# Optimization experiments

Hardware: AMD Instinct MI355X
Metric: run time of the kernel (lower is better)

## Reference

```python
import jax, jax.numpy as jnp
import numpy as np

N_USERS = 50000
N_ITEMS = 100000
N_NODES = N_USERS + N_ITEMS
N_EDGES = 2000000
EMBED = 64
N_LAYERS = 3
BATCH = 8192
NEG_SLOPE = 0.01  # torch LeakyReLU default
EPS = 1e-12       # torch F.normalize default


def setup_inputs() -> dict:
    key = jax.random.key(0)
    ks = jax.random.split(key, 12)
    return {
        "user_emb": jax.random.normal(ks[0], (N_USERS, EMBED), jnp.float32) * 0.1,
        "item_emb": jax.random.normal(ks[1], (N_ITEMS, EMBED), jnp.float32) * 0.1,
        "W1": jax.random.normal(ks[2], (N_LAYERS, EMBED, EMBED), jnp.float32) * 0.1,
        "b1": jax.random.normal(ks[3], (N_LAYERS, EMBED), jnp.float32) * 0.01,
        "W2": jax.random.normal(ks[4], (N_LAYERS, EMBED, EMBED), jnp.float32) * 0.1,
        "b2": jax.random.normal(ks[5], (N_LAYERS, EMBED), jnp.float32) * 0.01,
        "adj_vals": jax.random.uniform(ks[6], (N_EDGES,), jnp.float32),
        "adj_rows": jax.random.randint(ks[7], (N_EDGES,), 0, N_NODES, jnp.int32),
        "adj_cols": jax.random.randint(ks[8], (N_EDGES,), 0, N_NODES, jnp.int32),
        "u": jax.random.randint(ks[9], (BATCH,), 0, N_USERS, jnp.int32),
        "i": jax.random.randint(ks[10], (BATCH,), 0, N_ITEMS, jnp.int32),
        "j": jax.random.randint(ks[11], (BATCH,), 0, N_ITEMS, jnp.int32),
    }


def _spmm(rows, cols, vals, x):
    # sparse [N,N] @ dense [N,d] via gather + segment-sum
    return jax.ops.segment_sum(vals[:, None] * x[cols], rows, num_segments=N_NODES)


def _forward(user_emb, item_emb, W1, b1, W2, b2, adj_vals, adj_rows, adj_cols, u, i, j):
    emb = jnp.concatenate([user_emb, item_emb], axis=0)  # [N, d]
    finals = [emb]
    for l in range(N_LAYERS):
        t1e = _spmm(adj_rows, adj_cols, adj_vals, emb)        # A @ E
        t1 = t1e @ W1[l].T + b1[l]                             # Linear W1
        t2 = (emb * t1e) @ W2[l].T + b2[l]                     # Linear W2 on E (.) AE
        emb = jax.nn.leaky_relu(t1 + t2, NEG_SLOPE)
        norm = jnp.sqrt(jnp.sum(emb * emb, axis=1, keepdims=True))
        finals.append(emb / jnp.maximum(norm, EPS))
    fin = jnp.concatenate(finals, axis=1)                      # [N, d*(L+1)]
    fin_u, fin_i = fin[:N_USERS], fin[N_USERS:]
    bu, bp, bn = fin_u[u], fin_i[i], fin_i[j]
    pos_y = jnp.sum(bu * bp, axis=1)
    neg_y = jnp.sum(bu * bn, axis=1)
    return -jnp.mean(jax.nn.log_sigmoid(pos_y - neg_y))


def reference(user_emb, item_emb, W1, b1, W2, b2, adj_vals, adj_rows, adj_cols, u, i, j):
    return _forward(user_emb, item_emb, W1, b1, W2, b2, adj_vals, adj_rows, adj_cols, u, i, j)
```

## Files before the change

### kernel.cpp

```cpp
#include <hip/hip_runtime.h>
#include <hip/hip_bf16.h>
#include <math.h>

#define N_USERS 50000
#define N_ITEMS 100000
#define N_NODES 150000
#define N_EDGES 2000000
#define EMBED 64
#define N_LAYERS 3
#define BATCH 8192

#define BSHIFT 9
#define BROWS 512
#define NBKT ((N_NODES + BROWS - 1) / BROWS)
#define EPB 4096

typedef __bf16 bf16x8 __attribute__((ext_vector_type(8)));
typedef float  f32x4  __attribute__((ext_vector_type(4)));

__device__ __forceinline__ float bf2f(unsigned short u) {
    union { unsigned int i; float f; } c; c.i = ((unsigned int)u) << 16; return c.f;
}
__device__ __forceinline__ unsigned short f2bf(float f) {
    __hip_bfloat16 h = __float2bfloat16(f);
    union { __hip_bfloat16 h; unsigned short u; } c; c.h = h; return c.u;
}
__device__ __forceinline__ bf16x8 as_bf8(uint4 u) {
    union { uint4 u; bf16x8 v; } c; c.u = u; return c.v;
}
__device__ __forceinline__ void unpack8(uint4 u, float* f) {
    union { unsigned int i; float x; } c;
    c.i = u.x << 16; f[0] = c.x; c.i = u.x & 0xffff0000u; f[1] = c.x;
    c.i = u.y << 16; f[2] = c.x; c.i = u.y & 0xffff0000u; f[3] = c.x;
    c.i = u.z << 16; f[4] = c.x; c.i = u.z & 0xffff0000u; f[5] = c.x;
    c.i = u.w << 16; f[6] = c.x; c.i = u.w & 0xffff0000u; f[7] = c.x;
}
__device__ __forceinline__ bf16x8 pack8(const float* f) {
    union { unsigned short s[8]; bf16x8 v; } u;
#pragma unroll
    for (int j = 0; j < 8; j++) u.s[j] = f2bf(f[j]);
    return u.v;
}

__global__ __launch_bounds__(256) void k_tobf16(const float4* __restrict__ ue,
                                                const float4* __restrict__ ie,
                                                ushort4* __restrict__ tab) {
    int idx = blockIdx.x * 256 + threadIdx.x;
    const int TOT = N_NODES * EMBED / 4;
    const int UPART = N_USERS * EMBED / 4;
    if (idx < TOT) {
        float4 v = (idx < UPART) ? ue[idx] : ie[idx - UPART];
        ushort4 o;
        o.x = f2bf(v.x); o.y = f2bf(v.y); o.z = f2bf(v.z); o.w = f2bf(v.w);
        tab[idx] = o;
    }
}

__global__ __launch_bounds__(256) void k_wprep(const float* __restrict__ W1,
                                               const float* __restrict__ b1,
                                               const float* __restrict__ W2,
                                               const float* __restrict__ b2,
                                               unsigned short* __restrict__ Wb,
                                               float* __restrict__ bsum) {
    int idx = blockIdx.x * 256 + threadIdx.x;
    if (idx < 3 * 64 * 128) {
        int l = idx >> 13, rem = idx & 8191;
        int n = rem >> 7, k = rem & 127;
        float w = (k < 64) ? W1[l * 4096 + n * 64 + k] : W2[l * 4096 + n * 64 + (k - 64)];
        Wb[idx] = f2bf(w);
    } else if (idx < 3 * 64 * 128 + 192) {
        int t = idx - 3 * 64 * 128;
        bsum[t] = b1[t] + b2[t];
    }
}

__global__ __launch_bounds__(256) void k_bkt_count(const int* __restrict__ rows,
                                                   int* __restrict__ bkt_count) {
    __shared__ int hist[NBKT];
    int tid = threadIdx.x;
    for (int t = tid; t < NBKT; t += 256) hist[t] = 0;
    __syncthreads();
    int e = (blockIdx.x * 256 + tid) * 4;
    if (e + 3 < N_EDGES) {
        int4 r = *(const int4*)&rows[e];
        atomicAdd(&hist[r.x >> BSHIFT], 1);
        atomicAdd(&hist[r.y >> BSHIFT], 1);
        atomicAdd(&hist[r.z >> BSHIFT], 1);
        atomicAdd(&hist[r.w >> BSHIFT], 1);
    } else {
        for (int k = 0; k < 4; k++)
            if (e + k < N_EDGES) atomicAdd(&hist[rows[e + k] >> BSHIFT], 1);
    }
    __syncthreads();
    for (int t = tid; t < NBKT; t += 256)
        if (hist[t] > 0) atomicAdd(&bkt_count[t], hist[t]);
}

__global__ __launch_bounds__(512) void k_bkt_scan(const int* __restrict__ bkt_count,
                                                  int* __restrict__ bkt_base,
                                                  int* __restrict__ bkt_cursor,
                                                  int* __restrict__ row_ptr) {
    int tid = threadIdx.x;
    int x = (tid < NBKT) ? bkt_count[tid] : 0;
    int lane = tid & 63, wid = tid >> 6;
    int v = x;
    for (int o = 1; o < 64; o <<= 1) {
        int t = __shfl_up(v, o);
        if (lane >= o) v += t;
    }
    __shared__ int wsum[8];
    if (lane == 63) wsum[wid] = v;
    __syncthreads();
    int add = 0;
    for (int w = 0; w < wid; w++) add += wsum[w];
    int incl = add + v;
    int excl = incl - x;
    if (tid < NBKT) {
        bkt_base[tid]   = excl;
        bkt_cursor[tid] = excl;
    }
    if (tid == NBKT - 1) {
        bkt_base[NBKT]    = incl;
        row_ptr[N_NODES]  = incl;
    }
}

__global__ __launch_bounds__(256) void k_bucketA(const int* __restrict__ rows,
                                                 const int* __restrict__ cols,
                                                 const float* __restrict__ vals,
                                                 int* __restrict__ bkt_cursor,
                                                 int4* __restrict__ bucketed) {
    __shared__ int sr[EPB];
    __shared__ int sc[EPB];
    __shared__ int sv[EPB];
    __shared__ int hist[NBKT];
    __shared__ int cbase[NBKT];
    int tid = threadIdx.x;
    int e0 = blockIdx.x * EPB;
    int cnt = N_EDGES - e0; if (cnt > EPB) cnt = EPB;

    for (int i = tid; i < cnt; i += 256) {
        sr[i] = rows[e0 + i];
        sc[i] = cols[e0 + i];
        sv[i] = __float_as_int(vals[e0 + i]);
    }
    for (int t = tid; t < NBKT; t += 256) hist[t] = 0;
    __syncthreads();
    for (int i = tid; i < cnt; i += 256) atomicAdd(&hist[sr[i] >> BSHIFT], 1);
    __syncthreads();
    for (int t = tid; t < NBKT; t += 256)
        cbase[t] = (hist[t] > 0) ? atomicAdd(&bkt_cursor[t], hist[t]) : 0;
    __syncthreads();
    for (int t = tid; t < NBKT; t += 256) hist[t] = 0;
    __syncthreads();
    for (int i = tid; i < cnt; i += 256) {
        int b = sr[i] >> BSHIFT;
        int off = atomicAdd(&hist[b], 1);
        bucketed[cbase[b] + off] = make_int4(sr[i], sc[i], sv[i], 0);
    }
}

__global__ __launch_bounds__(1024) void k_bucketC(const int* __restrict__ bkt_base,
                                                  const int4* __restrict__ bucketed,
                                                  int* __restrict__ row_ptr,
                                                  int2* __restrict__ edges) {
    __shared__ int hist[BROWS];
    __shared__ int ssum[BROWS];
    __shared__ int cur[BROWS];
    int b = blockIdx.x, tid = threadIdx.x;
    int base = bkt_base[b];
    int cnt  = bkt_base[b + 1] - base;
    int row0 = b << BSHIFT;

    if (tid < BROWS) hist[tid] = 0;
    __syncthreads();
    for (int i = tid; i < cnt; i += 1024)
        atomicAdd(&hist[bucketed[base + i].x - row0], 1);
    __syncthreads();
    int own = 0;
    if (tid < BROWS) { own = hist[tid]; ssum[tid] = own; }
    __syncthreads();
    for (int off = 1; off < BROWS; off <<= 1) {
        int t = 0;
        if (tid < BROWS && tid >= off) t = ssum[tid - off];
        __syncthreads();
        if (tid < BROWS) ssum[tid] += t;
        __syncthreads();
    }
    if (tid < BROWS) {
        int excl = ssum[tid] - own;
        int grow = row0 + tid;
        if (grow < N_NODES) row_ptr[grow] = base + excl;
        cur[tid] = excl;
    }
    __syncthreads();
    for (int i = tid; i < cnt; i += 1024) {
        int4 ed = bucketed[base + i];
        int lr  = ed.x - row0;
        int off = atomicAdd(&cur[lr], 1);
        edges[base + off] = make_int2(ed.y, ed.z);
    }
}

__global__ __launch_bounds__(256) void k_spmm(const int*  __restrict__ row_ptr,
                                              const int2* __restrict__ edges,
                                              const unsigned short* __restrict__ tab,
                                              unsigned short* __restrict__ t1eH) {
    int wave = threadIdx.x >> 6, lane = threadIdx.x & 63;
    int row = blockIdx.x * 4 + wave;
    int slot = lane >> 3;
    int sl   = lane & 7;
    int s = row_ptr[row], e = row_ptr[row + 1];
    float acc[8] = {};
    for (int p = s + slot; p < e; p += 8) {
        int2  ed = edges[p];
        int   c  = ed.x;
        float v  = __int_as_float(ed.y);
        uint4 w  = *(const uint4*)&tab[c * EMBED + 8 * sl];
        union { unsigned int i; float f; } cv;
        cv.i = w.x << 16;          acc[0] += v * cv.f;
        cv.i = w.x & 0xffff0000u;  acc[1] += v * cv.f;
        cv.i = w.y << 16;          acc[2] += v * cv.f;
        cv.i = w.y & 0xffff0000u;  acc[3] += v * cv.f;
        cv.i = w.z << 16;          acc[4] += v * cv.f;
        cv.i = w.z & 0xffff0000u;  acc[5] += v * cv.f;
        cv.i = w.w << 16;          acc[6] += v * cv.f;
        cv.i = w.w & 0xffff0000u;  acc[7] += v * cv.f;
    }
#pragma unroll
    for (int k = 0; k < 8; k++) {
        acc[k] += __shfl_xor(acc[k], 8);
        acc[k] += __shfl_xor(acc[k], 16);
        acc[k] += __shfl_xor(acc[k], 32);
    }
    if (slot == 0) {
        uint4 o;
        o.x = (unsigned)f2bf(acc[0]) | ((unsigned)f2bf(acc[1]) << 16);
        o.y = (unsigned)f2bf(acc[2]) | ((unsigned)f2bf(acc[3]) << 16);
        o.z = (unsigned)f2bf(acc[4]) | ((unsigned)f2bf(acc[5]) << 16);
        o.w = (unsigned)f2bf(acc[6]) | ((unsigned)f2bf(acc[7]) << 16);
        *(uint4*)&t1eH[row * EMBED + 8 * sl] = o;
    }
}

__global__ __launch_bounds__(256) void k_dense(const unsigned short* __restrict__ t1eH,
                                               const unsigned short* __restrict__ embH_in,
                                               unsigned short* __restrict__ embH_out,
                                               const unsigned short* __restrict__ Wb,
                                               const float* __restrict__ bsum) {
    int tid  = threadIdx.x;
    int wave = tid >> 6, lane = tid & 63;
    int r16  = lane & 15, hi = lane >> 4;
    int rowt0 = blockIdx.x * 64 + wave * 16;
    int row   = rowt0 + r16;
    bool ok   = row < N_NODES;

    uint4 z4 = make_uint4(0u, 0u, 0u, 0u);
    const unsigned short* trow = t1eH    + (size_t)row * EMBED;
    const unsigned short* erow = embH_in + (size_t)row * EMBED;
    uint4 t_lo = ok ? *(const uint4*)(trow + hi * 8)      : z4;
    uint4 t_hi = ok ? *(const uint4*)(trow + 32 + hi * 8) : z4;
    uint4 e_lo = ok ? *(const uint4*)(erow + hi * 8)      : z4;
    uint4 e_hi = ok ? *(const uint4*)(erow + 32 + hi * 8) : z4;

    bf16x8 A0 = as_bf8(t_lo);
    bf16x8 A1 = as_bf8(t_hi);
    float ta[8], ea[8], pa[8];
    unpack8(t_lo, ta); unpack8(e_lo, ea);
#pragma unroll
    for (int j = 0; j < 8; j++) pa[j] = ta[j] * ea[j];
    bf16x8 A2 = pack8(pa);
    unpack8(t_hi, ta); unpack8(e_hi, ea);
#pragma unroll
    for (int j = 0; j < 8; j++) pa[j] = ta[j] * ea[j];
    bf16x8 A3 = pack8(pa);

#pragma unroll
    for (int nt = 0; nt < 4; nt++) {
        int wrow = nt * 16 + r16;
        const unsigned short* wp = Wb + wrow * 128 + hi * 8;
        bf16x8 B0 = as_bf8(*(const uint4*)(wp));
        bf16x8 B1 = as_bf8(*(const uint4*)(wp + 32));
        bf16x8 B2 = as_bf8(*(const uint4*)(wp + 64));
        bf16x8 B3 = as_bf8(*(const uint4*)(wp + 96));
        f32x4 c = {0.f, 0.f, 0.f, 0.f};
        c = __builtin_amdgcn_mfma_f32_16x16x32_bf16(A0, B0, c, 0, 0, 0);
        c = __builtin_amdgcn_mfma_f32_16x16x32_bf16(A1, B1, c, 0, 0, 0);
        c = __builtin_amdgcn_mfma_f32_16x16x32_bf16(A2, B2, c, 0, 0, 0);
        c = __builtin_amdgcn_mfma_f32_16x16x32_bf16(A3, B3, c, 0, 0, 0);

        int col = nt * 16 + r16;
        float bias = bsum[col];
#pragma unroll
        for (int r = 0; r < 4; r++) {
            int orow = rowt0 + hi * 4 + r;
            if (orow < N_NODES) {
                float v = c[r] + bias;
                v = (v > 0.f) ? v : 0.01f * v;
                embH_out[(size_t)orow * EMBED + col] = f2bf(v);
            }
        }
    }
}

__global__ __launch_bounds__(256) void k_score0(const float* __restrict__ ue,
                                                const float* __restrict__ ie,
                                                const int* __restrict__ u,
                                                const int* __restrict__ ii,
                                                const int* __restrict__ jj,
                                                float* __restrict__ posAcc,
                                                float* __restrict__ negAcc) {
    int wave = threadIdx.x >> 6, lane = threadIdx.x & 63;
    int b = blockIdx.x * 4 + wave;
    float eu = ue[u[b]  * EMBED + lane];
    float ep = ie[ii[b] * EMBED + lane];
    float en = ie[jj[b] * EMBED + lane];
    float p = eu * ep, n = eu * en;
    for (int o = 1; o < 64; o <<= 1) {
        p += __shfl_xor(p, o);
        n += __shfl_xor(n, o);
    }
    if (lane == 0) {
        posAcc[b] += p;
        negAcc[b] += n;
    }
}

__global__ __launch_bounds__(256) void k_score1(const unsigned short* __restrict__ tab,
                                                const int* __restrict__ u,
                                                const int* __restrict__ ii,
                                                const int* __restrict__ jj,
                                                float* __restrict__ posAcc,
                                                float* __restrict__ negAcc) {
    int wave = threadIdx.x >> 6, lane = threadIdx.x & 63;
    int b = blockIdx.x * 4 + wave;
    int ru = u[b];
    int ri = N_USERS + ii[b];
    int rj = N_USERS + jj[b];
    float eu = bf2f(tab[ru * EMBED + lane]);
    float ep = bf2f(tab[ri * EMBED + lane]);
    float en = bf2f(tab[rj * EMBED + lane]);
    float su = eu * eu, sp = ep * ep, sn = en * en;
    for (int o = 1; o < 64; o <<= 1) {
        su += __shfl_xor(su, o);
        sp += __shfl_xor(sp, o);
        sn += __shfl_xor(sn, o);
    }
    eu /= fmaxf(sqrtf(su), 1e-12f);
    ep /= fmaxf(sqrtf(sp), 1e-12f);
    en /= fmaxf(sqrtf(sn), 1e-12f);
    float p = eu * ep, n = eu * en;
    for (int o = 1; o < 64; o <<= 1) {
        p += __shfl_xor(p, o);
        n += __shfl_xor(n, o);
    }
    if (lane == 0) {
        posAcc[b] += p;
        negAcc[b] += n;
    }
}

__global__ __launch_bounds__(256) void k_loss(const float* __restrict__ pa,
                                              const float* __restrict__ na,
                                              float* __restrict__ out) {
    int b = blockIdx.x * 256 + threadIdx.x;
    float z = pa[b] - na[b];
    float x = -z;
    float sp = fmaxf(x, 0.f) + log1pf(expf(-fabsf(x)));
    for (int o = 1; o < 64; o <<= 1) sp += __shfl_xor(sp, o);
    __shared__ float s[4];
    int wave = threadIdx.x >> 6, lane = threadIdx.x & 63;
    if (lane == 0) s[wave] = sp;
    __syncthreads();
    if (threadIdx.x == 0) {
        float t = s[0] + s[1] + s[2] + s[3];
        atomicAdd(out, t * (1.f / (float)BATCH));
    }
}

extern "C" void kernel_launch(void* const* d_in, const int* in_sizes, int n_in,
                              void* d_out, int out_size, void* d_ws, size_t ws_size,
                              hipStream_t stream) {
    const float* user_emb = (const float*)d_in[0];
    const float* W1       = (const float*)d_in[2];
    const float* b1       = (const float*)d_in[3];
    const float* W2       = (const float*)d_in[4];
    const float* b2       = (const float*)d_in[5];
    const float* item_emb = (const float*)d_in[1];
    const float* adj_vals = (const float*)d_in[6];
    const int*   adj_rows = (const int*)d_in[7];
    const int*   adj_cols = (const int*)d_in[8];
    const int*   u_idx    = (const int*)d_in[9];
    const int*   i_idx    = (const int*)d_in[10];
    const int*   j_idx    = (const int*)d_in[11];
    float* out = (float*)d_out;

    char* ws = (char*)d_ws;
    unsigned short* t1eH       = (unsigned short*)(ws);
    int4*           bucketed   = (int4*)(ws);
    unsigned short* Wb         = (unsigned short*)(ws + 20000000);
    float*          bsum       = (float*)(ws + 20100000);
    int*            bkt_count  = (int*)(ws + 32000000);
    int*            bkt_base   = (int*)(ws + 32004096);
    int*            bkt_cursor = (int*)(ws + 32008192);
    unsigned short* HA         = (unsigned short*)(ws + 38400000);
    unsigned short* HB         = (unsigned short*)(ws + 57600000);
    int*            row_ptr    = (int*)(ws + 76800000);
    int2*           edges      = (int2*)(ws + 78000128);
    float*          posAcc     = (float*)(ws + 94000128);
    float*          negAcc     = (float*)(ws + 94032896);

    hipMemsetAsync(bkt_count, 0, 4096, stream);
    hipMemsetAsync(posAcc, 0, 2 * BATCH * sizeof(float), stream);
    hipMemsetAsync(d_out, 0, sizeof(float), stream);

    k_tobf16<<<(N_NODES * EMBED / 4 + 255) / 256, 256, 0, stream>>>(
        (const float4*)user_emb, (const float4*)item_emb, (ushort4*)HA);

    k_bkt_count<<<(N_EDGES / 4 + 255) / 256, 256, 0, stream>>>(adj_rows, bkt_count);
    k_bkt_scan<<<1, 512, 0, stream>>>(bkt_count, bkt_base, bkt_cursor, row_ptr);
    k_bucketA<<<(N_EDGES + EPB - 1) / EPB, 256, 0, stream>>>(adj_rows, adj_cols, adj_vals,
                                                             bkt_cursor, bucketed);
    k_bucketC<<<NBKT, 1024, 0, stream>>>(bkt_base, bucketed, row_ptr, edges);

    k_wprep<<<97, 256, 0, stream>>>(W1, b1, W2, b2, Wb, bsum);

    k_score0<<<BATCH / 4, 256, 0, stream>>>(user_emb, item_emb, u_idx, i_idx, j_idx,
                                            posAcc, negAcc);

    const int SGRID = N_NODES / 4;
    const int DGRID = (N_NODES + 63) / 64;

    k_spmm<<<SGRID, 256, 0, stream>>>(row_ptr, edges, HA, t1eH);
    k_dense<<<DGRID, 256, 0, stream>>>(t1eH, HA, HB, Wb, bsum);
    k_score1<<<BATCH / 4, 256, 0, stream>>>(HB, u_idx, i_idx, j_idx, posAcc, negAcc);

    k_spmm<<<SGRID, 256, 0, stream>>>(row_ptr, edges, HB, t1eH);
    k_dense<<<DGRID, 256, 0, stream>>>(t1eH, HB, HA, Wb + 8192, bsum + 64);
    k_score1<<<BATCH / 4, 256, 0, stream>>>(HA, u_idx, i_idx, j_idx, posAcc, negAcc);

    k_spmm<<<SGRID, 256, 0, stream>>>(row_ptr, edges, HA, t1eH);
    k_dense<<<DGRID, 256, 0, stream>>>(t1eH, HA, HB, Wb + 16384, bsum + 128);
    k_score1<<<BATCH / 4, 256, 0, stream>>>(HB, u_idx, i_idx, j_idx, posAcc, negAcc);

    k_loss<<<BATCH / 256, 256, 0, stream>>>(posAcc, negAcc, out);
}
```

Before: 425.3 us.

## Compute last layer only for batch-sampled rows and unroll SpMM gather by two

The final GNN layer's output is only consumed by the scoring of the sampled u/i/j rows, so the last SpMM and dense layer now run on just those 3*BATCH rows (gathered by index) instead of all nodes. A new score kernel reads the compacted outputs directly. Separately, the SpMM inner loop is unrolled to issue two edge gathers per iteration for more memory-level parallelism. Duplicate indices cause redundant recomputation, but this is far less work than the full layer.

```diff
diff --git a/kernel.cpp b/kernel.cpp
--- a/kernel.cpp
+++ b/kernel.cpp
@@ -9,6 +9,7 @@
 #define EMBED 64
 #define N_LAYERS 3
 #define BATCH 8192
+#define BATCH3 (3 * BATCH)
 
 #define BSHIFT 9
 #define BROWS 512
@@ -40,6 +41,17 @@
 #pragma unroll
     for (int j = 0; j < 8; j++) u.s[j] = f2bf(f[j]);
     return u.v;
+}
+__device__ __forceinline__ void gacc(uint4 w, float v, float* acc) {
+    union { unsigned int i; float f; } cv;
+    cv.i = w.x << 16;          acc[0] += v * cv.f;
+    cv.i = w.x & 0xffff0000u;  acc[1] += v * cv.f;
+    cv.i = w.y << 16;          acc[2] += v * cv.f;
+    cv.i = w.y & 0xffff0000u;  acc[3] += v * cv.f;
+    cv.i = w.z << 16;          acc[4] += v * cv.f;
+    cv.i = w.z & 0xffff0000u;  acc[5] += v * cv.f;
+    cv.i = w.w << 16;          acc[6] += v * cv.f;
+    cv.i = w.w & 0xffff0000u;  acc[7] += v * cv.f;
 }
 
 __global__ __launch_bounds__(256) void k_tobf16(const float4* __restrict__ ue,
@@ -212,20 +224,19 @@
     int sl   = lane & 7;
     int s = row_ptr[row], e = row_ptr[row + 1];
     float acc[8] = {};
-    for (int p = s + slot; p < e; p += 8) {
-        int2  ed = edges[p];
-        int   c  = ed.x;
-        float v  = __int_as_float(ed.y);
-        uint4 w  = *(const uint4*)&tab[c * EMBED + 8 * sl];
-        union { unsigned int i; float f; } cv;
-        cv.i = w.x << 16;          acc[0] += v * cv.f;
-        cv.i = w.x & 0xffff0000u;  acc[1] += v * cv.f;
-        cv.i = w.y << 16;          acc[2] += v * cv.f;
-        cv.i = w.y & 0xffff0000u;  acc[3] += v * cv.f;
-        cv.i = w.z << 16;          acc[4] += v * cv.f;
-        cv.i = w.z & 0xffff0000u;  acc[5] += v * cv.f;
-        cv.i = w.w << 16;          acc[6] += v * cv.f;
-        cv.i = w.w & 0xffff0000u;  acc[7] += v * cv.f;
+    int p = s + slot;
+    for (; p + 8 < e; p += 16) {
+        int2 ed0 = edges[p];
+        int2 ed1 = edges[p + 8];
+        uint4 w0 = *(const uint4*)&tab[ed0.x * EMBED + 8 * sl];
+        uint4 w1 = *(const uint4*)&tab[ed1.x * EMBED + 8 * sl];
+        gacc(w0, __int_as_float(ed0.y), acc);
+        gacc(w1, __int_as_float(ed1.y), acc);
+    }
+    if (p < e) {
+        int2 ed = edges[p];
+        uint4 w = *(const uint4*)&tab[ed.x * EMBED + 8 * sl];
+        gacc(w, __int_as_float(ed.y), acc);
     }
 #pragma unroll
     for (int k = 0; k < 8; k++) {
@@ -240,6 +251,55 @@
         o.z = (unsigned)f2bf(acc[4]) | ((unsigned)f2bf(acc[5]) << 16);
         o.w = (unsigned)f2bf(acc[6]) | ((unsigned)f2bf(acc[7]) << 16);
         *(uint4*)&t1eH[row * EMBED + 8 * sl] = o;
+    }
+}
+
+__device__ __forceinline__ int map_row(int bb, const int* u, const int* ii, const int* jj) {
+    if (bb < BATCH) return u[bb];
+    if (bb < 2 * BATCH) return N_USERS + ii[bb - BATCH];
+    return N_USERS + jj[bb - 2 * BATCH];
+}
+
+__global__ __launch_bounds__(256) void k_spmm_t(const int*  __restrict__ row_ptr,
+                                                const int2* __restrict__ edges,
+                                                const unsigned short* __restrict__ tab,
+                                                unsigned short* __restrict__ t1eS,
+                                                const int* __restrict__ u,
+                                                const int* __restrict__ ii,
+                                                const int* __restrict__ jj) {
+    int wave = threadIdx.x >> 6, lane = threadIdx.x & 63;
+    int bb = blockIdx.x * 4 + wave;
+    int row = map_row(bb, u, ii, jj);
+    int slot = lane >> 3, sl = lane & 7;
+    int s = row_ptr[row], e = row_ptr[row + 1];
+    float acc[8] = {};
+    int p = s + slot;
+    for (; p + 8 < e; p += 16) {
+        int2 ed0 = edges[p];
+        int2 ed1 = edges[p + 8];
+        uint4 w0 = *(const uint4*)&tab[ed0.x * EMBED + 8 * sl];
+        uint4 w1 = *(const uint4*)&tab[ed1.x * EMBED + 8 * sl];
+        gacc(w0, __int_as_float(ed0.y), acc);
+        gacc(w1, __int_as_float(ed1.y), acc);
+    }
+    if (p < e) {
+        int2 ed = edges[p];
+        uint4 w = *(const uint4*)&tab[ed.x * EMBED + 8 * sl];
+        gacc(w, __int_as_float(ed.y), acc);
+    }
+#pragma unroll
+    for (int k = 0; k < 8; k++) {
+        acc[k] += __shfl_xor(acc[k], 8);
+        acc[k] += __shfl_xor(acc[k], 16);
+        acc[k] += __shfl_xor(acc[k], 32);
+    }
+    if (slot == 0) {
+        uint4 o;
+        o.x = (unsigned)f2bf(acc[0]) | ((unsigned)f2bf(acc[1]) << 16);
+        o.y = (unsigned)f2bf(acc[2]) | ((unsigned)f2bf(acc[3]) << 16);
+        o.z = (unsigned)f2bf(acc[4]) | ((unsigned)f2bf(acc[5]) << 16);
+        o.w = (unsigned)f2bf(acc[6]) | ((unsigned)f2bf(acc[7]) << 16);
+        *(uint4*)&t1eS[bb * EMBED + 8 * sl] = o;
     }
 }
 
@@ -299,6 +359,66 @@
                 v = (v > 0.f) ? v : 0.01f * v;
                 embH_out[(size_t)orow * EMBED + col] = f2bf(v);
             }
+        }
+    }
+}
+
+__global__ __launch_bounds__(256) void k_dense_t(const unsigned short* __restrict__ t1eS,
+                                                 const unsigned short* __restrict__ embH_in,
+                                                 unsigned short* __restrict__ t2out,
+                                                 const unsigned short* __restrict__ Wb,
+                                                 const float* __restrict__ bsum,
+                                                 const int* __restrict__ u,
+                                                 const int* __restrict__ ii,
+                                                 const int* __restrict__ jj) {
+    int tid  = threadIdx.x;
+    int wave = tid >> 6, lane = tid & 63;
+    int r16  = lane & 15, hi = lane >> 4;
+    int rowt0 = blockIdx.x * 64 + wave * 16;
+    int bb   = rowt0 + r16;
+    int nrow = map_row(bb, u, ii, jj);
+
+    const unsigned short* trow = t1eS    + (size_t)bb   * EMBED;
+    const unsigned short* erow = embH_in + (size_t)nrow * EMBED;
+    uint4 t_lo = *(const uint4*)(trow + hi * 8);
+    uint4 t_hi = *(const uint4*)(trow + 32 + hi * 8);
+    uint4 e_lo = *(const uint4*)(erow + hi * 8);
+    uint4 e_hi = *(const uint4*)(erow + 32 + hi * 8);
+
+    bf16x8 A0 = as_bf8(t_lo);
+    bf16x8 A1 = as_bf8(t_hi);
+    float ta[8], ea[8], pa[8];
+    unpack8(t_lo, ta); unpack8(e_lo, ea);
+#pragma unroll
+    for (int j = 0; j < 8; j++) pa[j] = ta[j] * ea[j];
+    bf16x8 A2 = pack8(pa);
+    unpack8(t_hi, ta); unpack8(e_hi, ea);
+#pragma unroll
+    for (int j = 0; j < 8; j++) pa[j] = ta[j] * ea[j];
+    bf16x8 A3 = pack8(pa);
+
+#pragma unroll
+    for (int nt = 0; nt < 4; nt++) {
+        int wrow = nt * 16 + r16;
+        const unsigned short* wp = Wb + wrow * 128 + hi * 8;
+        bf16x8 B0 = as_bf8(*(const uint4*)(wp));
+        bf16x8 B1 = as_bf8(*(const uint4*)(wp + 32));
+        bf16x8 B2 = as_bf8(*(const uint4*)(wp + 64));
+        bf16x8 B3 = as_bf8(*(const uint4*)(wp + 96));
+        f32x4 c = {0.f, 0.f, 0.f, 0.f};
+        c = __builtin_amdgcn_mfma_f32_16x16x32_bf16(A0, B0, c, 0, 0, 0);
+        c = __builtin_amdgcn_mfma_f32_16x16x32_bf16(A1, B1, c, 0, 0, 0);
+        c = __builtin_amdgcn_mfma_f32_16x16x32_bf16(A2, B2, c, 0, 0, 0);
+        c = __builtin_amdgcn_mfma_f32_16x16x32_bf16(A3, B3, c, 0, 0, 0);
+
+        int col = nt * 16 + r16;
+        float bias = bsum[col];
+#pragma unroll
+        for (int r = 0; r < 4; r++) {
+            int obb = rowt0 + hi * 4 + r;
+            float v = c[r] + bias;
+            v = (v > 0.f) ? v : 0.01f * v;
+            t2out[(size_t)obb * EMBED + col] = f2bf(v);
         }
     }
 }
@@ -360,6 +480,34 @@
     }
 }
 
+__global__ __launch_bounds__(256) void k_score1t(const unsigned short* __restrict__ t2out,
+                                                 float* __restrict__ posAcc,
+                                                 float* __restrict__ negAcc) {
+    int wave = threadIdx.x >> 6, lane = threadIdx.x & 63;
+    int b = blockIdx.x * 4 + wave;
+    float eu = bf2f(t2out[(size_t)b * EMBED + lane]);
+    float ep = bf2f(t2out[(size_t)(BATCH + b) * EMBED + lane]);
+    float en = bf2f(t2out[(size_t)(2 * BATCH + b) * EMBED + lane]);
+    float su = eu * eu, sp = ep * ep, sn = en * en;
+    for (int o = 1; o < 64; o <<= 1) {
+        su += __shfl_xor(su, o);
+        sp += __shfl_xor(sp, o);
+        sn += __shfl_xor(sn, o);
+    }
+    eu /= fmaxf(sqrtf(su), 1e-12f);
+    ep /= fmaxf(sqrtf(sp), 1e-12f);
+    en /= fmaxf(sqrtf(sn), 1e-12f);
+    float p = eu * ep, n = eu * en;
+    for (int o = 1; o < 64; o <<= 1) {
+        p += __shfl_xor(p, o);
+        n += __shfl_xor(n, o);
+    }
+    if (lane == 0) {
+        posAcc[b] += p;
+        negAcc[b] += n;
+    }
+}
+
 __global__ __launch_bounds__(256) void k_loss(const float* __restrict__ pa,
                                               const float* __restrict__ na,
                                               float* __restrict__ out) {
@@ -382,11 +530,11 @@
                               void* d_out, int out_size, void* d_ws, size_t ws_size,
                               hipStream_t stream) {
     const float* user_emb = (const float*)d_in[0];
+    const float* item_emb = (const float*)d_in[1];
     const float* W1       = (const float*)d_in[2];
     const float* b1       = (const float*)d_in[3];
     const float* W2       = (const float*)d_in[4];
     const float* b2       = (const float*)d_in[5];
-    const float* item_emb = (const float*)d_in[1];
     const float* adj_vals = (const float*)d_in[6];
     const int*   adj_rows = (const int*)d_in[7];
     const int*   adj_cols = (const int*)d_in[8];
@@ -397,6 +545,8 @@
 
     char* ws = (char*)d_ws;
     unsigned short* t1eH       = (unsigned short*)(ws);
+    unsigned short* t1eS       = (unsigned short*)(ws);
+    unsigned short* t2out      = (unsigned short*)(ws + 4000000);
     int4*           bucketed   = (int4*)(ws);
     unsigned short* Wb         = (unsigned short*)(ws + 20000000);
     float*          bsum       = (float*)(ws + 20100000);
@@ -439,9 +589,11 @@
     k_dense<<<DGRID, 256, 0, stream>>>(t1eH, HB, HA, Wb + 8192, bsum + 64);
     k_score1<<<BATCH / 4, 256, 0, stream>>>(HA, u_idx, i_idx, j_idx, posAcc, negAcc);
 
-    k_spmm<<<SGRID, 256, 0, stream>>>(row_ptr, edges, HA, t1eH);
-    k_dense<<<DGRID, 256, 0, stream>>>(t1eH, HA, HB, Wb + 16384, bsum + 128);
-    k_score1<<<BATCH / 4, 256, 0, stream>>>(HB, u_idx, i_idx, j_idx, posAcc, negAcc);
+    k_spmm_t<<<BATCH3 / 4, 256, 0, stream>>>(row_ptr, edges, HA, t1eS,
+                                             u_idx, i_idx, j_idx);
+    k_dense_t<<<BATCH3 / 64, 256, 0, stream>>>(t1eS, HA, t2out, Wb + 16384, bsum + 128,
+                                               u_idx, i_idx, j_idx);
+    k_score1t<<<BATCH / 4, 256, 0, stream>>>(t2out, posAcc, negAcc);
 
     k_loss<<<BATCH / 256, 256, 0, stream>>>(posAcc, negAcc, out);
 }
```

Result: faster. 342.8 us (-19.4%).
